# Performance work log

Hardware: AMD Instinct MI355X
Metric: run time of the kernel (lower is better)

Reference implementation:

```python
import jax, jax.numpy as jnp
import numpy as np

N = 50000      # nodes
E = 800000     # edges (avg degree 16)
D_IN = 64
D_H = 128
D_OUT = 10
EPS = 1e-8


def setup_inputs() -> dict:
    key = jax.random.key(0)
    ks = jax.random.split(key, 6)
    x = jax.random.normal(ks[0], (N, D_IN), dtype=jnp.float32)
    edge_index = jax.random.randint(ks[1], (2, E), 0, N, dtype=jnp.int32)
    # weights act on homogeneous-augmented features (d_in + 1)
    W_self0 = jax.random.normal(ks[2], (D_IN + 1, D_H), jnp.float32) / np.sqrt(D_IN + 1)
    W_neigh0 = jax.random.normal(ks[3], (D_IN + 1, D_H), jnp.float32) / np.sqrt(D_IN + 1)
    W_self1 = jax.random.normal(ks[4], (D_H + 1, D_OUT), jnp.float32) / np.sqrt(D_H + 1)
    W_neigh1 = jax.random.normal(ks[5], (D_H + 1, D_OUT), jnp.float32) / np.sqrt(D_H + 1)
    return {"x": x, "edge_index": edge_index,
            "W_self0": W_self0, "W_neigh0": W_neigh0,
            "W_self1": W_self1, "W_neigh1": W_neigh1}


def _projective_sage_layer(h, src, dst, W_self, W_neigh, last):
    n = h.shape[0]
    # lift to projective (homogeneous) coordinates: append ones column
    hh = jnp.concatenate([h, jnp.ones((n, 1), h.dtype)], axis=1)  # [N, d+1]
    # mean-aggregate neighbor messages (irregular gather + segment-sum)
    msg_sum = jax.ops.segment_sum(hh[src], dst, num_segments=n)   # [N, d+1]
    deg = jax.ops.segment_sum(jnp.ones((src.shape[0],), h.dtype), dst, num_segments=n)
    neigh = msg_sum / jnp.maximum(deg, 1.0)[:, None]
    out = hh @ W_self + neigh @ W_neigh                           # [N, d_out]
    # projective normalization (points on unit sphere of projective space)
    out = out / (jnp.linalg.norm(out, axis=1, keepdims=True) + EPS)
    return out if last else jax.nn.relu(out)


def reference(x, edge_index, W_self0, W_neigh0, W_self1, W_neigh1):
    src, dst = edge_index[0], edge_index[1]
    h = _projective_sage_layer(x, src, dst, W_self0, W_neigh0, last=False)
    h = _projective_sage_layer(h, src, dst, W_self1, W_neigh1, last=True)
    return jax.nn.log_softmax(h, axis=1)
```

## Files before the change

### kernel.cpp

```cpp
#include <hip/hip_runtime.h>
#include <hip/hip_bf16.h>
#include <math.h>

#define EPSN 1e-8f
#define MAXBUCK 512

typedef __attribute__((ext_vector_type(8))) short short8;
typedef __attribute__((ext_vector_type(4))) float f32x4;

static __device__ __forceinline__ unsigned short f2bf(float f) {
    union { float f; unsigned int u; } v; v.f = f;
    unsigned int u = v.u;
    return (unsigned short)((u + 0x7fffu + ((u >> 16) & 1u)) >> 16);
}
static __device__ __forceinline__ float bf2f(unsigned short h) {
    union { unsigned int u; float f; } v; v.u = ((unsigned int)h) << 16;
    return v.f;
}

__global__ void fused_pre(const int* __restrict__ dst, int* __restrict__ ghist, int E, int nbuck,
                          const float* __restrict__ Ws0, const float* __restrict__ Wn0,
                          const float* __restrict__ Ws1, const float* __restrict__ Wn1,
                          unsigned short* __restrict__ B0t, unsigned short* __restrict__ B1t,
                          float* __restrict__ bias,
                          const float* __restrict__ x, unsigned short* __restrict__ A0, int N,
                          int histB, int prepB) {
    int b = blockIdx.x;
    if (b < histB) {
        __shared__ int h[MAXBUCK];
        for (int i = threadIdx.x; i < MAXBUCK; i += 256) h[i] = 0;
        __syncthreads();
        int CH = (E + histB - 1) / histB;
        int lo = b * CH, hi = min(E, lo + CH);
        for (int e = lo + (int)threadIdx.x; e < hi; e += 256) atomicAdd(&h[dst[e] >> 7], 1);
        __syncthreads();
        for (int i = threadIdx.x; i < nbuck; i += 256) if (h[i]) atomicAdd(&ghist[i], h[i]);
        return;
    }
    if (b < histB + prepB) {
        int t = (b - histB) * 256 + threadIdx.x;
        if (t < 128 * 160) {
            int n = t / 160, k = t % 160;
            float v = 0.f;
            if (k < 64) v = Ws0[k * 128 + n];
            else if (k < 128) v = Wn0[(k - 64) * 128 + n];
            else if (k == 128) v = Ws0[64 * 128 + n];
            else if (k == 129) v = Wn0[64 * 128 + n];
            B0t[n * 160 + k] = f2bf(v);
        }
        int u = t - 128 * 160;
        if (u >= 0 && u < 32 * 128) {
            int c = u / 128, k = u % 128;
            float v = 0.f;
            if (c < 10) v = Ws1[k * 10 + c];
            else if (c < 20) v = Wn1[k * 10 + (c - 10)];
            B1t[c * 128 + k] = f2bf(v);
        }
        int w = t - 128 * 160 - 32 * 128;
        if (w >= 0 && w < 20) bias[w] = (w < 10) ? Ws1[128 * 10 + w] : Wn1[128 * 10 + (w - 10)];
        return;
    }
    int u = (b - histB - prepB) * 256 + threadIdx.x;
    if (u >= N * 8) return;
    int n = u >> 3, s = u & 7;
    const float4* xp = (const float4*)(x + (size_t)n * 64 + s * 8);
    float4 v0 = xp[0], v1 = xp[1];
    short8 r;
    r[0] = (short)f2bf(v0.x); r[1] = (short)f2bf(v0.y);
    r[2] = (short)f2bf(v0.z); r[3] = (short)f2bf(v0.w);
    r[4] = (short)f2bf(v1.x); r[5] = (short)f2bf(v1.y);
    r[6] = (short)f2bf(v1.z); r[7] = (short)f2bf(v1.w);
    *(short8*)(&A0[(size_t)n * 160 + s * 8]) = r;
}

__global__ void bucket_scan(const int* __restrict__ ghist, int* __restrict__ boff,
                            int* __restrict__ bcur, int nbuck, int E,
                            int* __restrict__ row_ptr, int N) {
    __shared__ int bufa[MAXBUCK], bufb[MAXBUCK];
    int t = threadIdx.x;
    int v = (t < nbuck) ? ghist[t] : 0;
    bufa[t] = v;
    __syncthreads();
    int* cur = bufa; int* nxt = bufb;
    for (int off = 1; off < MAXBUCK; off <<= 1) {
        int xv = cur[t];
        if (t >= off) xv += cur[t - off];
        nxt[t] = xv;
        __syncthreads();
        int* tmp = cur; cur = nxt; nxt = tmp;
    }
    int incl = cur[t];
    int excl = incl - v;
    if (t < nbuck) { boff[t] = excl; bcur[t] = excl; }
    if (t == nbuck - 1) boff[nbuck] = incl;
    if (t == 0) row_ptr[N] = E;
}

__global__ void bucket_scatter(const int* __restrict__ src, const int* __restrict__ dst,
                               int* __restrict__ bcur, unsigned int* __restrict__ pairs,
                               int E) {
    __shared__ int h[MAXBUCK];
    __shared__ int bs[MAXBUCK];
    for (int i = threadIdx.x; i < MAXBUCK; i += 256) h[i] = 0;
    __syncthreads();
    int CH = (E + gridDim.x - 1) / gridDim.x;
    int lo = blockIdx.x * CH, hi = min(E, lo + CH);
    for (int e = lo + (int)threadIdx.x; e < hi; e += 256) atomicAdd(&h[dst[e] >> 7], 1);
    __syncthreads();
    for (int i = threadIdx.x; i < MAXBUCK; i += 256) {
        int c = h[i];
        bs[i] = c ? atomicAdd(&bcur[i], c) : 0;
        h[i] = 0;
    }
    __syncthreads();
    for (int e = lo + (int)threadIdx.x; e < hi; e += 256) {
        int d = dst[e];
        int b = d >> 7;
        int idx = atomicAdd(&h[b], 1);
        pairs[bs[b] + idx] = (((unsigned int)(d & 127)) << 16) | (unsigned int)src[e];
    }
}

__global__ void csr_finalize(const unsigned int* __restrict__ pairs, const int* __restrict__ boff,
                             int* __restrict__ row_ptr, unsigned short* __restrict__ col,
                             int N) {
    __shared__ int lh[128], ls[128], lc[128];
    int b = blockIdx.x, t = threadIdx.x;
    int lo = boff[b], hi = boff[b + 1];
    for (int i = t; i < 128; i += 256) lh[i] = 0;
    __syncthreads();
    for (int e = lo + t; e < hi; e += 256) atomicAdd(&lh[pairs[e] >> 16], 1);
    __syncthreads();
    if (t < 128) {
        int v = lh[t];
        int incl = v;
#pragma unroll
        for (int off = 1; off < 64; off <<= 1) {
            int y = __shfl_up(incl, off);
            if ((t & 63) >= off) incl += y;
        }
        ls[t] = incl;
    }
    __syncthreads();
    if (t < 128) {
        int v = lh[t];
        int excl = ls[t] - v + ((t >= 64) ? ls[63] : 0);
        int node = b * 128 + t;
        if (node < N) row_ptr[node] = lo + excl;
        lc[t] = excl;
    }
    __syncthreads();
    for (int e = lo + t; e < hi; e += 256) {
        unsigned int p = pairs[e];
        int ld = p >> 16;
        int idx = atomicAdd(&lc[ld], 1);
        col[lo + idx] = (unsigned short)(p & 0xFFFFu);
    }
}

#define ACC4(v) { a0 += bf2f((unsigned short)((v).x & 0xFFFFu)); \
                  a1 += bf2f((unsigned short)((v).x >> 16)); \
                  a2 += bf2f((unsigned short)((v).y & 0xFFFFu)); \
                  a3 += bf2f((unsigned short)((v).y >> 16)); }

__global__ void agg0_kernel(const int* __restrict__ row_ptr, const unsigned short* __restrict__ col,
                            unsigned short* __restrict__ A0, int N) {
    int n = (int)((blockIdx.x * blockDim.x + threadIdx.x) >> 6);
    if (n >= N) return;
    int lane = threadIdx.x & 63;
    int sub = lane >> 4, f = lane & 15;
    int rs = row_ptr[n], re = row_ptr[n + 1];
    float a0 = 0.f, a1 = 0.f, a2 = 0.f, a3 = 0.f;
    for (int base = rs; base < re; base += 64) {
        int cnt = min(64, re - base);
        int e = 0;
        if (base + lane < re) e = (int)col[base + lane];
        int j = 0;
        for (; j + 16 <= cnt; j += 16) {
            int s0 = __shfl(e, j + sub);
            int s1 = __shfl(e, j + 4 + sub);
            int s2 = __shfl(e, j + 8 + sub);
            int s3 = __shfl(e, j + 12 + sub);
            uint2 v0 = *(const uint2*)(&A0[(size_t)s0 * 160 + f * 4]);
            uint2 v1 = *(const uint2*)(&A0[(size_t)s1 * 160 + f * 4]);
            uint2 v2 = *(const uint2*)(&A0[(size_t)s2 * 160 + f * 4]);
            uint2 v3 = *(const uint2*)(&A0[(size_t)s3 * 160 + f * 4]);
            ACC4(v0); ACC4(v1); ACC4(v2); ACC4(v3);
        }
        for (; j < cnt; j += 4) {
            int idx = j + sub;
            int s = __shfl(e, idx < cnt ? idx : (cnt - 1));
            if (idx < cnt) {
                uint2 v = *(const uint2*)(&A0[(size_t)s * 160 + f * 4]);
                ACC4(v);
            }
        }
    }
    a0 += __shfl_xor(a0, 16); a0 += __shfl_xor(a0, 32);
    a1 += __shfl_xor(a1, 16); a1 += __shfl_xor(a1, 32);
    a2 += __shfl_xor(a2, 16); a2 += __shfl_xor(a2, 32);
    a3 += __shfl_xor(a3, 16); a3 += __shfl_xor(a3, 32);
    float deg = (float)(re - rs);
    float scale = 1.0f / fmaxf(deg, 1.0f);
    unsigned short* row = A0 + (size_t)n * 160;
    if (sub == 0) {
        uint2 o;
        o.x = ((unsigned int)f2bf(a1 * scale) << 16) | f2bf(a0 * scale);
        o.y = ((unsigned int)f2bf(a3 * scale) << 16) | f2bf(a2 * scale);
        *(uint2*)(&row[64 + f * 4]) = o;
    } else if (sub == 1) {
        unsigned int w = (f == 0) ? ((((unsigned int)f2bf(deg * scale)) << 16) | 0x3F80u) : 0u;
        *(unsigned int*)(&row[128 + f * 2]) = w;
    }
}

__global__ void __launch_bounds__(256)
gemm0_kernel(const unsigned short* __restrict__ A0, const unsigned short* __restrict__ B0t,
             unsigned short* __restrict__ h1, int N) {
    __shared__ unsigned short As[64 * 168];
    __shared__ unsigned short Bs[128 * 168];
    int t = threadIdx.x, blk = blockIdx.x;
    for (int i = t; i < 128 * 20; i += 256) {
        int r = i / 20, c = i % 20;
        *(uint4*)(&Bs[r * 168 + c * 8]) = *(const uint4*)(&B0t[r * 160 + c * 8]);
    }
    for (int i = t; i < 64 * 20; i += 256) {
        int r = i / 20, c = i % 20;
        int gr = blk * 64 + r;
        uint4 v = {0, 0, 0, 0};
        if (gr < N) v = *(const uint4*)(&A0[(size_t)gr * 160 + c * 8]);
        *(uint4*)(&As[r * 168 + c * 8]) = v;
    }
    __syncthreads();

    int wave = t >> 6, lane = t & 63;
    int lo = lane & 15, hi = lane >> 4;
    f32x4 acc[8];
#pragma unroll
    for (int f = 0; f < 8; ++f) acc[f] = (f32x4){0.f, 0.f, 0.f, 0.f};

#pragma unroll
    for (int ks = 0; ks < 5; ++ks) {
        short8 a = *(const short8*)(&As[(wave * 16 + lo) * 168 + ks * 32 + hi * 8]);
#pragma unroll
        for (int f = 0; f < 8; ++f) {
            short8 b = *(const short8*)(&Bs[(f * 16 + lo) * 168 + ks * 32 + hi * 8]);
            acc[f] = __builtin_amdgcn_mfma_f32_16x16x32_bf16(a, b, acc[f], 0, 0, 0);
        }
    }
#pragma unroll
    for (int j = 0; j < 4; ++j) {
        float s = 0.f;
#pragma unroll
        for (int f = 0; f < 8; ++f) s += acc[f][j] * acc[f][j];
#pragma unroll
        for (int m = 1; m < 16; m <<= 1) s += __shfl_xor(s, m);
        float inv = 1.0f / (sqrtf(s) + EPSN);
        int gr = blk * 64 + wave * 16 + hi * 4 + j;
        if (gr < N) {
#pragma unroll
            for (int f = 0; f < 8; ++f)
                h1[(size_t)gr * 128 + f * 16 + lo] = f2bf(fmaxf(acc[f][j] * inv, 0.f));
        }
    }
}

__global__ void __launch_bounds__(256)
gemm1_kernel(const unsigned short* __restrict__ h1, const unsigned short* __restrict__ B1t,
             const float* __restrict__ bias, float* __restrict__ S, float* __restrict__ Qp, int N) {
    __shared__ unsigned short As[128 * 136];
    __shared__ unsigned short Bs[32 * 136];
    int t = threadIdx.x, blk = blockIdx.x;
    for (int i = t; i < 32 * 16; i += 256) {
        int r = i / 16, c = i % 16;
        *(uint4*)(&Bs[r * 136 + c * 8]) = *(const uint4*)(&B1t[r * 128 + c * 8]);
    }
    for (int i = t; i < 128 * 16; i += 256) {
        int r = i / 16, c = i % 16;
        int gr = blk * 128 + r;
        uint4 v = {0, 0, 0, 0};
        if (gr < N) v = *(const uint4*)(&h1[(size_t)gr * 128 + c * 8]);
        *(uint4*)(&As[r * 136 + c * 8]) = v;
    }
    __syncthreads();

    int wave = t >> 6, lane = t & 63, lo = lane & 15, hi = lane >> 4;
    f32x4 acc[2][2];
#pragma unroll
    for (int m = 0; m < 2; ++m) { acc[m][0] = (f32x4){0,0,0,0}; acc[m][1] = (f32x4){0,0,0,0}; }

#pragma unroll
    for (int ks = 0; ks < 4; ++ks) {
        short8 b0 = *(const short8*)(&Bs[lo * 136 + ks * 32 + hi * 8]);
        short8 b1 = *(const short8*)(&Bs[(16 + lo) * 136 + ks * 32 + hi * 8]);
#pragma unroll
        for (int m = 0; m < 2; ++m) {
            short8 a = *(const short8*)(&As[(wave * 32 + m * 16 + lo) * 136 + ks * 32 + hi * 8]);
            acc[m][0] = __builtin_amdgcn_mfma_f32_16x16x32_bf16(a, b0, acc[m][0], 0, 0, 0);
            acc[m][1] = __builtin_amdgcn_mfma_f32_16x16x32_bf16(a, b1, acc[m][1], 0, 0, 0);
        }
    }
#pragma unroll
    for (int m = 0; m < 2; ++m)
#pragma unroll
        for (int j = 0; j < 4; ++j) {
            int gr = blk * 128 + wave * 32 + m * 16 + hi * 4 + j;
            if (gr < N) {
                float v0 = acc[m][0][j] + bias[lo];
                if (lo < 10) S[(size_t)gr * 10 + lo] = v0;
                else         Qp[(size_t)gr * 16 + (lo - 10)] = v0;
                if (lo < 4)       Qp[(size_t)gr * 16 + 6 + lo] = acc[m][1][j] + bias[16 + lo];
                else if (lo < 10) Qp[(size_t)gr * 16 + 6 + lo] = 0.f;
            }
        }
}

__global__ void final_kernel(const float* __restrict__ S, const float* __restrict__ Qp,
                             const int* __restrict__ row_ptr, const unsigned short* __restrict__ col,
                             float* __restrict__ out, int N) {
    int n = (int)((blockIdx.x * blockDim.x + threadIdx.x) >> 6);
    if (n >= N) return;
    int lane = threadIdx.x & 63;
    int sub = lane >> 4, f = lane & 15;
    int rs = row_ptr[n], re = row_ptr[n + 1];
    float qx = 0.f, qy = 0.f;
    for (int base = rs; base < re; base += 64) {
        int cnt = min(64, re - base);
        int e = 0;
        if (base + lane < re) e = (int)col[base + lane];
        int j = 0;
        for (; j + 16 <= cnt; j += 16) {
            int s0 = __shfl(e, j + sub);
            int s1 = __shfl(e, j + 4 + sub);
            int s2 = __shfl(e, j + 8 + sub);
            int s3 = __shfl(e, j + 12 + sub);
            if (f < 8) {
                float2 v0 = *(const float2*)(&Qp[(size_t)s0 * 16 + f * 2]);
                float2 v1 = *(const float2*)(&Qp[(size_t)s1 * 16 + f * 2]);
                float2 v2 = *(const float2*)(&Qp[(size_t)s2 * 16 + f * 2]);
                float2 v3 = *(const float2*)(&Qp[(size_t)s3 * 16 + f * 2]);
                qx += v0.x + v1.x + v2.x + v3.x;
                qy += v0.y + v1.y + v2.y + v3.y;
            }
        }
        for (; j < cnt; j += 4) {
            int idx = j + sub;
            int s = __shfl(e, idx < cnt ? idx : (cnt - 1));
            if (idx < cnt && f < 8) {
                float2 v = *(const float2*)(&Qp[(size_t)s * 16 + f * 2]);
                qx += v.x; qy += v.y;
            }
        }
    }
    qx += __shfl_xor(qx, 16); qx += __shfl_xor(qx, 32);
    qy += __shfl_xor(qy, 16); qy += __shfl_xor(qy, 32);
    float deg = (float)(re - rs);
    float scale = 1.0f / fmaxf(deg, 1.0f);
    float px = 0.f, py = 0.f;
    if (f < 5) {
        px = S[(size_t)n * 10 + 2 * f]     + qx * scale;
        py = S[(size_t)n * 10 + 2 * f + 1] + qy * scale;
    }
    float ss = px * px + py * py;
    ss += __shfl_xor(ss, 1); ss += __shfl_xor(ss, 2);
    ss += __shfl_xor(ss, 4); ss += __shfl_xor(ss, 8);
    float inv = 1.0f / (sqrtf(ss) + EPSN);
    px *= inv; py *= inv;
    float mx = (f < 5) ? fmaxf(px, py) : -INFINITY;
    mx = fmaxf(mx, __shfl_xor(mx, 1)); mx = fmaxf(mx, __shfl_xor(mx, 2));
    mx = fmaxf(mx, __shfl_xor(mx, 4)); mx = fmaxf(mx, __shfl_xor(mx, 8));
    float se = (f < 5) ? (expf(px - mx) + expf(py - mx)) : 0.f;
    se += __shfl_xor(se, 1); se += __shfl_xor(se, 2);
    se += __shfl_xor(se, 4); se += __shfl_xor(se, 8);
    float ls = logf(se) + mx;
    if (sub == 0 && f < 5) {
        out[(size_t)n * 10 + 2 * f]     = px - ls;
        out[(size_t)n * 10 + 2 * f + 1] = py - ls;
    }
}

extern "C" void kernel_launch(void* const* d_in, const int* in_sizes, int n_in,
                              void* d_out, int out_size, void* d_ws, size_t ws_size,
                              hipStream_t stream) {
    const float* x   = (const float*)d_in[0];
    const int*   ei  = (const int*)d_in[1];
    const float* Ws0 = (const float*)d_in[2];
    const float* Wn0 = (const float*)d_in[3];
    const float* Ws1 = (const float*)d_in[4];
    const float* Wn1 = (const float*)d_in[5];

    int N = in_sizes[0] / 64;
    int E = in_sizes[1] / 2;
    const int* src = ei;
    const int* dst = ei + E;
    int nbuck = (N + 127) / 128;

    char* ws = (char*)d_ws;
    size_t off = 0;
    unsigned short* A0   = (unsigned short*)(ws + off); off += (size_t)N * 160 * 2;
    unsigned short* h1   = (unsigned short*)(ws + off); off += (size_t)N * 128 * 2;
    float*          S    = (float*)(ws + off);          off += (size_t)N * 10 * 4;
    float*          Qp   = (float*)(ws + off);          off += (size_t)N * 16 * 4;
    unsigned short* B0t  = (unsigned short*)(ws + off); off += 128 * 160 * 2;
    unsigned short* B1t  = (unsigned short*)(ws + off); off += 32 * 128 * 2;
    float*          bias = (float*)(ws + off);          off += 128;
    int*            rowp = (int*)(ws + off);            off += ((size_t)N + 4) * 4;
    unsigned short* colb = (unsigned short*)(ws + off); off += ((size_t)E + 8) * 2;
    unsigned int*   pairs= (unsigned int*)(ws + off);   off += (size_t)E * 4;
    int*            ghist= (int*)(ws + off);            off += MAXBUCK * 4;
    int*            boff = (int*)(ws + off);            off += (MAXBUCK + 1) * 4;
    int*            bcur = (int*)(ws + off);            off += MAXBUCK * 4;
    float* outp = (float*)d_out;

    int histB = 256;
    int prepB = (128 * 160 + 32 * 128 + 20 + 255) / 256;
    int xcvB  = (N * 8 + 255) / 256;

    hipMemsetAsync(ghist, 0, MAXBUCK * 4, stream);
    fused_pre<<<histB + prepB + xcvB, 256, 0, stream>>>(
        dst, ghist, E, nbuck, Ws0, Wn0, Ws1, Wn1, B0t, B1t, bias, x, A0, N, histB, prepB);
    bucket_scan   <<<1, MAXBUCK, 0, stream>>>(ghist, boff, bcur, nbuck, E, rowp, N);
    bucket_scatter<<<256, 256, 0, stream>>>(src, dst, bcur, pairs, E);
    csr_finalize  <<<nbuck, 256, 0, stream>>>(pairs, boff, rowp, colb, N);

    agg0_kernel <<<(N + 3) / 4, 256, 0, stream>>>(rowp, colb, A0, N);
    gemm0_kernel<<<(N + 63) / 64, 256, 0, stream>>>(A0, B0t, h1, N);
    gemm1_kernel<<<(N + 127) / 128, 256, 0, stream>>>(h1, B1t, bias, S, Qp, N);
    final_kernel<<<(N + 3) / 4, 256, 0, stream>>>(S, Qp, rowp, colb, outp, N);
}
```

Measured before the change: 186.7 us.

## Fuse all stages into one cooperative persistent kernel with grid syncs

Replaces the eight separate kernel launches (histogram, scan, scatter, CSR finalize, aggregation, two GEMMs, final softmax) with one cooperative kernel of 256 blocks by 512 threads that runs each stage as a grid-stride loop separated by grid.sync(). This removes the per-launch overhead and the gaps between launches. Per-stage work mappings are also reorganised, for example 8-row groups per wave in the final aggregation and split output columns with a shared-memory norm reduction in GEMM0. In exchange, parallelism is capped at 256 persistent blocks, and every grid barrier waits on the slowest block, which can leave compute units idle during the irregular gather stages.

```diff
diff --git a/kernel.cpp b/kernel.cpp
--- a/kernel.cpp
+++ b/kernel.cpp
@@ -1,9 +1,13 @@
 #include <hip/hip_runtime.h>
-#include <hip/hip_bf16.h>
+#include <hip/hip_cooperative_groups.h>
 #include <math.h>
+
+namespace cg = cooperative_groups;
 
 #define EPSN 1e-8f
 #define MAXBUCK 512
+#define NB 256
+#define NT 512
 
 typedef __attribute__((ext_vector_type(8))) short short8;
 typedef __attribute__((ext_vector_type(4))) float f32x4;
@@ -17,365 +21,367 @@
     union { unsigned int u; float f; } v; v.u = ((unsigned int)h) << 16;
     return v.f;
 }
-
-__global__ void fused_pre(const int* __restrict__ dst, int* __restrict__ ghist, int E, int nbuck,
-                          const float* __restrict__ Ws0, const float* __restrict__ Wn0,
-                          const float* __restrict__ Ws1, const float* __restrict__ Wn1,
-                          unsigned short* __restrict__ B0t, unsigned short* __restrict__ B1t,
-                          float* __restrict__ bias,
-                          const float* __restrict__ x, unsigned short* __restrict__ A0, int N,
-                          int histB, int prepB) {
-    int b = blockIdx.x;
-    if (b < histB) {
-        __shared__ int h[MAXBUCK];
-        for (int i = threadIdx.x; i < MAXBUCK; i += 256) h[i] = 0;
-        __syncthreads();
-        int CH = (E + histB - 1) / histB;
-        int lo = b * CH, hi = min(E, lo + CH);
-        for (int e = lo + (int)threadIdx.x; e < hi; e += 256) atomicAdd(&h[dst[e] >> 7], 1);
-        __syncthreads();
-        for (int i = threadIdx.x; i < nbuck; i += 256) if (h[i]) atomicAdd(&ghist[i], h[i]);
-        return;
-    }
-    if (b < histB + prepB) {
-        int t = (b - histB) * 256 + threadIdx.x;
-        if (t < 128 * 160) {
-            int n = t / 160, k = t % 160;
-            float v = 0.f;
-            if (k < 64) v = Ws0[k * 128 + n];
-            else if (k < 128) v = Wn0[(k - 64) * 128 + n];
-            else if (k == 128) v = Ws0[64 * 128 + n];
-            else if (k == 129) v = Wn0[64 * 128 + n];
-            B0t[n * 160 + k] = f2bf(v);
-        }
-        int u = t - 128 * 160;
-        if (u >= 0 && u < 32 * 128) {
-            int c = u / 128, k = u % 128;
-            float v = 0.f;
-            if (c < 10) v = Ws1[k * 10 + c];
-            else if (c < 20) v = Wn1[k * 10 + (c - 10)];
-            B1t[c * 128 + k] = f2bf(v);
-        }
-        int w = t - 128 * 160 - 32 * 128;
-        if (w >= 0 && w < 20) bias[w] = (w < 10) ? Ws1[128 * 10 + w] : Wn1[128 * 10 + (w - 10)];
-        return;
-    }
-    int u = (b - histB - prepB) * 256 + threadIdx.x;
-    if (u >= N * 8) return;
-    int n = u >> 3, s = u & 7;
-    const float4* xp = (const float4*)(x + (size_t)n * 64 + s * 8);
-    float4 v0 = xp[0], v1 = xp[1];
-    short8 r;
-    r[0] = (short)f2bf(v0.x); r[1] = (short)f2bf(v0.y);
-    r[2] = (short)f2bf(v0.z); r[3] = (short)f2bf(v0.w);
-    r[4] = (short)f2bf(v1.x); r[5] = (short)f2bf(v1.y);
-    r[6] = (short)f2bf(v1.z); r[7] = (short)f2bf(v1.w);
-    *(short8*)(&A0[(size_t)n * 160 + s * 8]) = r;
+static __device__ __forceinline__ unsigned int pk2(float a, float b) {
+    return (((unsigned int)f2bf(b)) << 16) | (unsigned int)f2bf(a);
 }
 
-__global__ void bucket_scan(const int* __restrict__ ghist, int* __restrict__ boff,
-                            int* __restrict__ bcur, int nbuck, int E,
-                            int* __restrict__ row_ptr, int N) {
-    __shared__ int bufa[MAXBUCK], bufb[MAXBUCK];
-    int t = threadIdx.x;
-    int v = (t < nbuck) ? ghist[t] : 0;
-    bufa[t] = v;
-    __syncthreads();
-    int* cur = bufa; int* nxt = bufb;
-    for (int off = 1; off < MAXBUCK; off <<= 1) {
-        int xv = cur[t];
-        if (t >= off) xv += cur[t - off];
-        nxt[t] = xv;
-        __syncthreads();
-        int* tmp = cur; cur = nxt; nxt = tmp;
-    }
-    int incl = cur[t];
-    int excl = incl - v;
-    if (t < nbuck) { boff[t] = excl; bcur[t] = excl; }
-    if (t == nbuck - 1) boff[nbuck] = incl;
-    if (t == 0) row_ptr[N] = E;
-}
-
-__global__ void bucket_scatter(const int* __restrict__ src, const int* __restrict__ dst,
-                               int* __restrict__ bcur, unsigned int* __restrict__ pairs,
-                               int E) {
-    __shared__ int h[MAXBUCK];
-    __shared__ int bs[MAXBUCK];
-    for (int i = threadIdx.x; i < MAXBUCK; i += 256) h[i] = 0;
-    __syncthreads();
-    int CH = (E + gridDim.x - 1) / gridDim.x;
-    int lo = blockIdx.x * CH, hi = min(E, lo + CH);
-    for (int e = lo + (int)threadIdx.x; e < hi; e += 256) atomicAdd(&h[dst[e] >> 7], 1);
-    __syncthreads();
-    for (int i = threadIdx.x; i < MAXBUCK; i += 256) {
-        int c = h[i];
-        bs[i] = c ? atomicAdd(&bcur[i], c) : 0;
-        h[i] = 0;
-    }
-    __syncthreads();
-    for (int e = lo + (int)threadIdx.x; e < hi; e += 256) {
-        int d = dst[e];
-        int b = d >> 7;
-        int idx = atomicAdd(&h[b], 1);
-        pairs[bs[b] + idx] = (((unsigned int)(d & 127)) << 16) | (unsigned int)src[e];
-    }
-}
-
-__global__ void csr_finalize(const unsigned int* __restrict__ pairs, const int* __restrict__ boff,
-                             int* __restrict__ row_ptr, unsigned short* __restrict__ col,
-                             int N) {
-    __shared__ int lh[128], ls[128], lc[128];
-    int b = blockIdx.x, t = threadIdx.x;
-    int lo = boff[b], hi = boff[b + 1];
-    for (int i = t; i < 128; i += 256) lh[i] = 0;
-    __syncthreads();
-    for (int e = lo + t; e < hi; e += 256) atomicAdd(&lh[pairs[e] >> 16], 1);
-    __syncthreads();
-    if (t < 128) {
-        int v = lh[t];
-        int incl = v;
-#pragma unroll
-        for (int off = 1; off < 64; off <<= 1) {
-            int y = __shfl_up(incl, off);
-            if ((t & 63) >= off) incl += y;
-        }
-        ls[t] = incl;
-    }
-    __syncthreads();
-    if (t < 128) {
-        int v = lh[t];
-        int excl = ls[t] - v + ((t >= 64) ? ls[63] : 0);
-        int node = b * 128 + t;
-        if (node < N) row_ptr[node] = lo + excl;
-        lc[t] = excl;
-    }
-    __syncthreads();
-    for (int e = lo + t; e < hi; e += 256) {
-        unsigned int p = pairs[e];
-        int ld = p >> 16;
-        int idx = atomicAdd(&lc[ld], 1);
-        col[lo + idx] = (unsigned short)(p & 0xFFFFu);
-    }
-}
-
-#define ACC4(v) { a0 += bf2f((unsigned short)((v).x & 0xFFFFu)); \
-                  a1 += bf2f((unsigned short)((v).x >> 16)); \
-                  a2 += bf2f((unsigned short)((v).y & 0xFFFFu)); \
-                  a3 += bf2f((unsigned short)((v).y >> 16)); }
-
-__global__ void agg0_kernel(const int* __restrict__ row_ptr, const unsigned short* __restrict__ col,
-                            unsigned short* __restrict__ A0, int N) {
-    int n = (int)((blockIdx.x * blockDim.x + threadIdx.x) >> 6);
-    if (n >= N) return;
-    int lane = threadIdx.x & 63;
-    int sub = lane >> 4, f = lane & 15;
-    int rs = row_ptr[n], re = row_ptr[n + 1];
-    float a0 = 0.f, a1 = 0.f, a2 = 0.f, a3 = 0.f;
-    for (int base = rs; base < re; base += 64) {
-        int cnt = min(64, re - base);
-        int e = 0;
-        if (base + lane < re) e = (int)col[base + lane];
-        int j = 0;
-        for (; j + 16 <= cnt; j += 16) {
-            int s0 = __shfl(e, j + sub);
-            int s1 = __shfl(e, j + 4 + sub);
-            int s2 = __shfl(e, j + 8 + sub);
-            int s3 = __shfl(e, j + 12 + sub);
-            uint2 v0 = *(const uint2*)(&A0[(size_t)s0 * 160 + f * 4]);
-            uint2 v1 = *(const uint2*)(&A0[(size_t)s1 * 160 + f * 4]);
-            uint2 v2 = *(const uint2*)(&A0[(size_t)s2 * 160 + f * 4]);
-            uint2 v3 = *(const uint2*)(&A0[(size_t)s3 * 160 + f * 4]);
-            ACC4(v0); ACC4(v1); ACC4(v2); ACC4(v3);
-        }
-        for (; j < cnt; j += 4) {
-            int idx = j + sub;
-            int s = __shfl(e, idx < cnt ? idx : (cnt - 1));
-            if (idx < cnt) {
-                uint2 v = *(const uint2*)(&A0[(size_t)s * 160 + f * 4]);
-                ACC4(v);
-            }
-        }
-    }
-    a0 += __shfl_xor(a0, 16); a0 += __shfl_xor(a0, 32);
-    a1 += __shfl_xor(a1, 16); a1 += __shfl_xor(a1, 32);
-    a2 += __shfl_xor(a2, 16); a2 += __shfl_xor(a2, 32);
-    a3 += __shfl_xor(a3, 16); a3 += __shfl_xor(a3, 32);
-    float deg = (float)(re - rs);
-    float scale = 1.0f / fmaxf(deg, 1.0f);
-    unsigned short* row = A0 + (size_t)n * 160;
-    if (sub == 0) {
-        uint2 o;
-        o.x = ((unsigned int)f2bf(a1 * scale) << 16) | f2bf(a0 * scale);
-        o.y = ((unsigned int)f2bf(a3 * scale) << 16) | f2bf(a2 * scale);
-        *(uint2*)(&row[64 + f * 4]) = o;
-    } else if (sub == 1) {
-        unsigned int w = (f == 0) ? ((((unsigned int)f2bf(deg * scale)) << 16) | 0x3F80u) : 0u;
-        *(unsigned int*)(&row[128 + f * 2]) = w;
-    }
-}
-
-__global__ void __launch_bounds__(256)
-gemm0_kernel(const unsigned short* __restrict__ A0, const unsigned short* __restrict__ B0t,
-             unsigned short* __restrict__ h1, int N) {
-    __shared__ unsigned short As[64 * 168];
-    __shared__ unsigned short Bs[128 * 168];
-    int t = threadIdx.x, blk = blockIdx.x;
-    for (int i = t; i < 128 * 20; i += 256) {
-        int r = i / 20, c = i % 20;
-        *(uint4*)(&Bs[r * 168 + c * 8]) = *(const uint4*)(&B0t[r * 160 + c * 8]);
-    }
-    for (int i = t; i < 64 * 20; i += 256) {
-        int r = i / 20, c = i % 20;
-        int gr = blk * 64 + r;
-        uint4 v = {0, 0, 0, 0};
-        if (gr < N) v = *(const uint4*)(&A0[(size_t)gr * 160 + c * 8]);
-        *(uint4*)(&As[r * 168 + c * 8]) = v;
-    }
-    __syncthreads();
-
-    int wave = t >> 6, lane = t & 63;
-    int lo = lane & 15, hi = lane >> 4;
-    f32x4 acc[8];
-#pragma unroll
-    for (int f = 0; f < 8; ++f) acc[f] = (f32x4){0.f, 0.f, 0.f, 0.f};
-
-#pragma unroll
-    for (int ks = 0; ks < 5; ++ks) {
-        short8 a = *(const short8*)(&As[(wave * 16 + lo) * 168 + ks * 32 + hi * 8]);
-#pragma unroll
-        for (int f = 0; f < 8; ++f) {
-            short8 b = *(const short8*)(&Bs[(f * 16 + lo) * 168 + ks * 32 + hi * 8]);
-            acc[f] = __builtin_amdgcn_mfma_f32_16x16x32_bf16(a, b, acc[f], 0, 0, 0);
-        }
-    }
-#pragma unroll
-    for (int j = 0; j < 4; ++j) {
-        float s = 0.f;
-#pragma unroll
-        for (int f = 0; f < 8; ++f) s += acc[f][j] * acc[f][j];
-#pragma unroll
-        for (int m = 1; m < 16; m <<= 1) s += __shfl_xor(s, m);
-        float inv = 1.0f / (sqrtf(s) + EPSN);
-        int gr = blk * 64 + wave * 16 + hi * 4 + j;
-        if (gr < N) {
-#pragma unroll
-            for (int f = 0; f < 8; ++f)
-                h1[(size_t)gr * 128 + f * 16 + lo] = f2bf(fmaxf(acc[f][j] * inv, 0.f));
-        }
-    }
-}
-
-__global__ void __launch_bounds__(256)
-gemm1_kernel(const unsigned short* __restrict__ h1, const unsigned short* __restrict__ B1t,
-             const float* __restrict__ bias, float* __restrict__ S, float* __restrict__ Qp, int N) {
-    __shared__ unsigned short As[128 * 136];
-    __shared__ unsigned short Bs[32 * 136];
-    int t = threadIdx.x, blk = blockIdx.x;
-    for (int i = t; i < 32 * 16; i += 256) {
-        int r = i / 16, c = i % 16;
-        *(uint4*)(&Bs[r * 136 + c * 8]) = *(const uint4*)(&B1t[r * 128 + c * 8]);
-    }
-    for (int i = t; i < 128 * 16; i += 256) {
-        int r = i / 16, c = i % 16;
-        int gr = blk * 128 + r;
-        uint4 v = {0, 0, 0, 0};
-        if (gr < N) v = *(const uint4*)(&h1[(size_t)gr * 128 + c * 8]);
-        *(uint4*)(&As[r * 136 + c * 8]) = v;
-    }
-    __syncthreads();
-
-    int wave = t >> 6, lane = t & 63, lo = lane & 15, hi = lane >> 4;
-    f32x4 acc[2][2];
-#pragma unroll
-    for (int m = 0; m < 2; ++m) { acc[m][0] = (f32x4){0,0,0,0}; acc[m][1] = (f32x4){0,0,0,0}; }
-
-#pragma unroll
-    for (int ks = 0; ks < 4; ++ks) {
-        short8 b0 = *(const short8*)(&Bs[lo * 136 + ks * 32 + hi * 8]);
-        short8 b1 = *(const short8*)(&Bs[(16 + lo) * 136 + ks * 32 + hi * 8]);
-#pragma unroll
-        for (int m = 0; m < 2; ++m) {
-            short8 a = *(const short8*)(&As[(wave * 32 + m * 16 + lo) * 136 + ks * 32 + hi * 8]);
-            acc[m][0] = __builtin_amdgcn_mfma_f32_16x16x32_bf16(a, b0, acc[m][0], 0, 0, 0);
-            acc[m][1] = __builtin_amdgcn_mfma_f32_16x16x32_bf16(a, b1, acc[m][1], 0, 0, 0);
-        }
-    }
-#pragma unroll
-    for (int m = 0; m < 2; ++m)
-#pragma unroll
-        for (int j = 0; j < 4; ++j) {
-            int gr = blk * 128 + wave * 32 + m * 16 + hi * 4 + j;
-            if (gr < N) {
-                float v0 = acc[m][0][j] + bias[lo];
-                if (lo < 10) S[(size_t)gr * 10 + lo] = v0;
-                else         Qp[(size_t)gr * 16 + (lo - 10)] = v0;
-                if (lo < 4)       Qp[(size_t)gr * 16 + 6 + lo] = acc[m][1][j] + bias[16 + lo];
-                else if (lo < 10) Qp[(size_t)gr * 16 + 6 + lo] = 0.f;
-            }
-        }
-}
-
-__global__ void final_kernel(const float* __restrict__ S, const float* __restrict__ Qp,
-                             const int* __restrict__ row_ptr, const unsigned short* __restrict__ col,
-                             float* __restrict__ out, int N) {
-    int n = (int)((blockIdx.x * blockDim.x + threadIdx.x) >> 6);
-    if (n >= N) return;
-    int lane = threadIdx.x & 63;
-    int sub = lane >> 4, f = lane & 15;
-    int rs = row_ptr[n], re = row_ptr[n + 1];
-    float qx = 0.f, qy = 0.f;
-    for (int base = rs; base < re; base += 64) {
-        int cnt = min(64, re - base);
-        int e = 0;
-        if (base + lane < re) e = (int)col[base + lane];
-        int j = 0;
-        for (; j + 16 <= cnt; j += 16) {
-            int s0 = __shfl(e, j + sub);
-            int s1 = __shfl(e, j + 4 + sub);
-            int s2 = __shfl(e, j + 8 + sub);
-            int s3 = __shfl(e, j + 12 + sub);
-            if (f < 8) {
-                float2 v0 = *(const float2*)(&Qp[(size_t)s0 * 16 + f * 2]);
-                float2 v1 = *(const float2*)(&Qp[(size_t)s1 * 16 + f * 2]);
-                float2 v2 = *(const float2*)(&Qp[(size_t)s2 * 16 + f * 2]);
-                float2 v3 = *(const float2*)(&Qp[(size_t)s3 * 16 + f * 2]);
-                qx += v0.x + v1.x + v2.x + v3.x;
-                qy += v0.y + v1.y + v2.y + v3.y;
-            }
-        }
-        for (; j < cnt; j += 4) {
-            int idx = j + sub;
-            int s = __shfl(e, idx < cnt ? idx : (cnt - 1));
-            if (idx < cnt && f < 8) {
-                float2 v = *(const float2*)(&Qp[(size_t)s * 16 + f * 2]);
-                qx += v.x; qy += v.y;
-            }
-        }
-    }
-    qx += __shfl_xor(qx, 16); qx += __shfl_xor(qx, 32);
-    qy += __shfl_xor(qy, 16); qy += __shfl_xor(qy, 32);
-    float deg = (float)(re - rs);
-    float scale = 1.0f / fmaxf(deg, 1.0f);
-    float px = 0.f, py = 0.f;
-    if (f < 5) {
-        px = S[(size_t)n * 10 + 2 * f]     + qx * scale;
-        py = S[(size_t)n * 10 + 2 * f + 1] + qy * scale;
-    }
-    float ss = px * px + py * py;
-    ss += __shfl_xor(ss, 1); ss += __shfl_xor(ss, 2);
-    ss += __shfl_xor(ss, 4); ss += __shfl_xor(ss, 8);
-    float inv = 1.0f / (sqrtf(ss) + EPSN);
-    px *= inv; py *= inv;
-    float mx = (f < 5) ? fmaxf(px, py) : -INFINITY;
-    mx = fmaxf(mx, __shfl_xor(mx, 1)); mx = fmaxf(mx, __shfl_xor(mx, 2));
-    mx = fmaxf(mx, __shfl_xor(mx, 4)); mx = fmaxf(mx, __shfl_xor(mx, 8));
-    float se = (f < 5) ? (expf(px - mx) + expf(py - mx)) : 0.f;
-    se += __shfl_xor(se, 1); se += __shfl_xor(se, 2);
-    se += __shfl_xor(se, 4); se += __shfl_xor(se, 8);
-    float ls = logf(se) + mx;
-    if (sub == 0 && f < 5) {
-        out[(size_t)n * 10 + 2 * f]     = px - ls;
-        out[(size_t)n * 10 + 2 * f + 1] = py - ls;
+struct MegaParams {
+    const float* x; const int* src; const int* dst;
+    const float* Ws0; const float* Wn0; const float* Ws1; const float* Wn1;
+    unsigned short* A0; unsigned short* h1; float* S; float* Qp;
+    unsigned short* B0t; unsigned short* B1t; float* bias;
+    int* rowp; unsigned short* colb; unsigned int* pairs;
+    int* ghist; int* boff; int* bcur;
+    float* out; int N; int E; int nbuck;
+};
+
+#define ACC8(v) { a0 += bf2f((unsigned short)((v).x & 0xFFFFu)); a1 += bf2f((unsigned short)((v).x >> 16)); \
+                  a2 += bf2f((unsigned short)((v).y & 0xFFFFu)); a3 += bf2f((unsigned short)((v).y >> 16)); \
+                  a4 += bf2f((unsigned short)((v).z & 0xFFFFu)); a5 += bf2f((unsigned short)((v).z >> 16)); \
+                  a6 += bf2f((unsigned short)((v).w & 0xFFFFu)); a7 += bf2f((unsigned short)((v).w >> 16)); }
+
+__global__ void __launch_bounds__(NT, 2) mega_kernel(MegaParams p) {
+    cg::grid_group grid = cg::this_grid();
+    __shared__ __align__(16) char smem[64512];
+    const int tid = threadIdx.x;
+    const int bid = blockIdx.x;
+    const int w = tid >> 6, lane = tid & 63;
+
+    {
+        int* h = (int*)smem;
+        for (int i = tid; i < MAXBUCK; i += NT) h[i] = 0;
+        __syncthreads();
+        int CH = (p.E + NB - 1) / NB;
+        int lo = bid * CH, hi = min(p.E, lo + CH);
+        for (int e = lo + tid; e < hi; e += NT) atomicAdd(&h[p.dst[e] >> 7], 1);
+        __syncthreads();
+        for (int i = tid; i < p.nbuck; i += NT) { int c = h[i]; if (c) atomicAdd(&p.ghist[i], c); }
+
+        for (int u = bid * NT + tid; u < p.N * 8; u += NB * NT) {
+            int n = u >> 3, s = u & 7;
+            const float4* xp = (const float4*)(p.x + (size_t)n * 64 + s * 8);
+            float4 v0 = xp[0], v1 = xp[1];
+            short8 r;
+            r[0] = (short)f2bf(v0.x); r[1] = (short)f2bf(v0.y);
+            r[2] = (short)f2bf(v0.z); r[3] = (short)f2bf(v0.w);
+            r[4] = (short)f2bf(v1.x); r[5] = (short)f2bf(v1.y);
+            r[6] = (short)f2bf(v1.z); r[7] = (short)f2bf(v1.w);
+            *(short8*)(&p.A0[(size_t)n * 160 + s * 8]) = r;
+        }
+        const int PT = 128 * 160 + 32 * 128 + 20;
+        for (int t = bid * NT + tid; t < PT; t += NB * NT) {
+            if (t < 128 * 160) {
+                int n = t / 160, k = t % 160;
+                float v = 0.f;
+                if (k < 64) v = p.Ws0[k * 128 + n];
+                else if (k < 128) v = p.Wn0[(k - 64) * 128 + n];
+                else if (k == 128) v = p.Ws0[64 * 128 + n];
+                else if (k == 129) v = p.Wn0[64 * 128 + n];
+                p.B0t[n * 160 + k] = f2bf(v);
+            } else if (t < 128 * 160 + 32 * 128) {
+                int u2 = t - 128 * 160;
+                int c = u2 / 128, k = u2 % 128;
+                float v = 0.f;
+                if (c < 10) v = p.Ws1[k * 10 + c];
+                else if (c < 20) v = p.Wn1[k * 10 + (c - 10)];
+                p.B1t[c * 128 + k] = f2bf(v);
+            } else {
+                int w2 = t - 128 * 160 - 32 * 128;
+                p.bias[w2] = (w2 < 10) ? p.Ws1[128 * 10 + w2] : p.Wn1[128 * 10 + (w2 - 10)];
+            }
+        }
+    }
+    grid.sync();
+
+    if (bid == 0) {
+        int* bufa = (int*)smem; int* bufb = bufa + MAXBUCK;
+        int t = tid;
+        int v = (t < p.nbuck) ? p.ghist[t] : 0;
+        bufa[t] = v;
+        __syncthreads();
+        int* cur = bufa; int* nxt = bufb;
+        for (int off2 = 1; off2 < MAXBUCK; off2 <<= 1) {
+            int xv = cur[t];
+            if (t >= off2) xv += cur[t - off2];
+            nxt[t] = xv;
+            __syncthreads();
+            int* tmp = cur; cur = nxt; nxt = tmp;
+        }
+        int incl = cur[t], excl = incl - v;
+        if (t < p.nbuck) { p.boff[t] = excl; p.bcur[t] = excl; }
+        if (t == p.nbuck - 1) p.boff[p.nbuck] = incl;
+        if (t == 0) p.rowp[p.N] = p.E;
+    }
+    grid.sync();
+
+    {
+        int* h = (int*)smem; int* bs = h + MAXBUCK;
+        for (int i = tid; i < MAXBUCK; i += NT) h[i] = 0;
+        __syncthreads();
+        int CH = (p.E + NB - 1) / NB;
+        int lo = bid * CH, hi = min(p.E, lo + CH);
+        for (int e = lo + tid; e < hi; e += NT) atomicAdd(&h[p.dst[e] >> 7], 1);
+        __syncthreads();
+        for (int i = tid; i < MAXBUCK; i += NT) {
+            int c = h[i];
+            bs[i] = c ? atomicAdd(&p.bcur[i], c) : 0;
+            h[i] = 0;
+        }
+        __syncthreads();
+        for (int e = lo + tid; e < hi; e += NT) {
+            int d = p.dst[e];
+            int b = d >> 7;
+            int idx = atomicAdd(&h[b], 1);
+            p.pairs[bs[b] + idx] = (((unsigned int)(d & 127)) << 16) | (unsigned int)p.src[e];
+        }
+    }
+    grid.sync();
+
+    for (int b = bid; b < p.nbuck; b += NB) {
+        int* lh = (int*)smem; int* ls = lh + 128; int* lc = ls + 128;
+        int lo = p.boff[b], hi = p.boff[b + 1];
+        for (int i = tid; i < 128; i += NT) lh[i] = 0;
+        __syncthreads();
+        for (int e = lo + tid; e < hi; e += NT) atomicAdd(&lh[p.pairs[e] >> 16], 1);
+        __syncthreads();
+        if (tid < 128) {
+            int v = lh[tid];
+            int incl = v;
+#pragma unroll
+            for (int off2 = 1; off2 < 64; off2 <<= 1) {
+                int y = __shfl_up(incl, off2);
+                if ((tid & 63) >= off2) incl += y;
+            }
+            ls[tid] = incl;
+        }
+        __syncthreads();
+        if (tid < 128) {
+            int v = lh[tid];
+            int excl = ls[tid] - v + ((tid >= 64) ? ls[63] : 0);
+            int node = b * 128 + tid;
+            if (node < p.N) p.rowp[node] = lo + excl;
+            lc[tid] = excl;
+        }
+        __syncthreads();
+        for (int e = lo + tid; e < hi; e += NT) {
+            unsigned int pr = p.pairs[e];
+            int ld = pr >> 16;
+            int idx = atomicAdd(&lc[ld], 1);
+            p.colb[lo + idx] = (unsigned short)(pr & 0xFFFFu);
+        }
+        __syncthreads();
+    }
+    grid.sync();
+
+    {
+        int sub = lane >> 3, f8 = lane & 7;
+        for (int n = bid * 8 + w; n < p.N; n += NB * 8) {
+            int rs = p.rowp[n], re = p.rowp[n + 1];
+            float a0 = 0.f, a1 = 0.f, a2 = 0.f, a3 = 0.f, a4 = 0.f, a5 = 0.f, a6 = 0.f, a7 = 0.f;
+            for (int base = rs; base < re; base += 64) {
+                int cnt = min(64, re - base);
+                int e = 0;
+                if (base + lane < re) e = (int)p.colb[base + lane];
+                int j = 0;
+                for (; j + 32 <= cnt; j += 32) {
+                    int s0 = __shfl(e, j + sub);
+                    int s1 = __shfl(e, j + 8 + sub);
+                    int s2 = __shfl(e, j + 16 + sub);
+                    int s3 = __shfl(e, j + 24 + sub);
+                    uint4 v0 = *(const uint4*)(&p.A0[(size_t)s0 * 160 + f8 * 8]);
+                    uint4 v1 = *(const uint4*)(&p.A0[(size_t)s1 * 160 + f8 * 8]);
+                    uint4 v2 = *(const uint4*)(&p.A0[(size_t)s2 * 160 + f8 * 8]);
+                    uint4 v3 = *(const uint4*)(&p.A0[(size_t)s3 * 160 + f8 * 8]);
+                    ACC8(v0); ACC8(v1); ACC8(v2); ACC8(v3);
+                }
+                for (; j < cnt; j += 8) {
+                    int idx = j + sub;
+                    int s = __shfl(e, idx < cnt ? idx : (cnt - 1));
+                    if (idx < cnt) {
+                        uint4 v = *(const uint4*)(&p.A0[(size_t)s * 160 + f8 * 8]);
+                        ACC8(v);
+                    }
+                }
+            }
+#define RED8(a) { a += __shfl_xor(a, 8); a += __shfl_xor(a, 16); a += __shfl_xor(a, 32); }
+            RED8(a0); RED8(a1); RED8(a2); RED8(a3); RED8(a4); RED8(a5); RED8(a6); RED8(a7);
+            float deg = (float)(re - rs);
+            float scale = 1.0f / fmaxf(deg, 1.0f);
+            if (sub == 0) {
+                uint4 o;
+                o.x = pk2(a0 * scale, a1 * scale);
+                o.y = pk2(a2 * scale, a3 * scale);
+                o.z = pk2(a4 * scale, a5 * scale);
+                o.w = pk2(a6 * scale, a7 * scale);
+                *(uint4*)(&p.A0[(size_t)n * 160 + 64 + f8 * 8]) = o;
+            } else if (sub == 1) {
+                uint2 z = {0u, 0u};
+                if (f8 == 0) z.x = ((unsigned int)f2bf(deg * scale) << 16) | 0x3F80u;
+                *(uint2*)(&p.A0[(size_t)n * 160 + 128 + f8 * 4]) = z;
+            }
+        }
+    }
+    grid.sync();
+
+    {
+        unsigned short* Bs = (unsigned short*)smem;
+        unsigned short* As = Bs + 128 * 168;
+        for (int i = tid; i < 128 * 20; i += NT) {
+            int r = i / 20, c = i % 20;
+            *(uint4*)(&Bs[r * 168 + c * 8]) = *(const uint4*)(&p.B0t[r * 160 + c * 8]);
+        }
+        __syncthreads();
+        int lo16 = lane & 15, hi4 = lane >> 4;
+        int rw = w >> 1, fh = w & 1;
+        int ntile = (p.N + 63) >> 6;
+        for (int tile = bid; tile < ntile; tile += NB) {
+            for (int i = tid; i < 64 * 20; i += NT) {
+                int r = i / 20, c = i % 20;
+                int gr = tile * 64 + r;
+                uint4 v = {0, 0, 0, 0};
+                if (gr < p.N) v = *(const uint4*)(&p.A0[(size_t)gr * 160 + c * 8]);
+                *(uint4*)(&As[r * 168 + c * 8]) = v;
+            }
+            __syncthreads();
+            f32x4 acc[4];
+#pragma unroll
+            for (int f = 0; f < 4; ++f) acc[f] = (f32x4){0.f, 0.f, 0.f, 0.f};
+#pragma unroll
+            for (int ks = 0; ks < 5; ++ks) {
+                short8 a = *(const short8*)(&As[(rw * 16 + lo16) * 168 + ks * 32 + hi4 * 8]);
+#pragma unroll
+                for (int f = 0; f < 4; ++f) {
+                    short8 b = *(const short8*)(&Bs[((fh * 4 + f) * 16 + lo16) * 168 + ks * 32 + hi4 * 8]);
+                    acc[f] = __builtin_amdgcn_mfma_f32_16x16x32_bf16(a, b, acc[f], 0, 0, 0);
+                }
+            }
+            __syncthreads();
+            float* sred = (float*)As;
+#pragma unroll
+            for (int j = 0; j < 4; ++j) {
+                float s = 0.f;
+#pragma unroll
+                for (int f = 0; f < 4; ++f) s += acc[f][j] * acc[f][j];
+#pragma unroll
+                for (int m = 1; m < 16; m <<= 1) s += __shfl_xor(s, m);
+                if (lo16 == 0) sred[fh * 64 + rw * 16 + hi4 * 4 + j] = s;
+            }
+            __syncthreads();
+#pragma unroll
+            for (int j = 0; j < 4; ++j) {
+                int rit = rw * 16 + hi4 * 4 + j;
+                float stot = sred[rit] + sred[64 + rit];
+                float inv = 1.0f / (sqrtf(stot) + EPSN);
+                int gr = tile * 64 + rit;
+                if (gr < p.N) {
+#pragma unroll
+                    for (int f = 0; f < 4; ++f)
+                        p.h1[(size_t)gr * 128 + (fh * 4 + f) * 16 + lo16] = f2bf(fmaxf(acc[f][j] * inv, 0.f));
+                }
+            }
+            __syncthreads();
+        }
+    }
+    grid.sync();
+
+    {
+        unsigned short* Bs = (unsigned short*)smem;
+        unsigned short* As = Bs + 32 * 136;
+        for (int i = tid; i < 32 * 16; i += NT) {
+            int r = i / 16, c = i % 16;
+            *(uint4*)(&Bs[r * 136 + c * 8]) = *(const uint4*)(&p.B1t[r * 128 + c * 8]);
+        }
+        __syncthreads();
+        int lo16 = lane & 15, hi4 = lane >> 4;
+        int ntile = (p.N + 127) >> 7;
+        for (int tile = bid; tile < ntile; tile += NB) {
+            for (int i = tid; i < 128 * 16; i += NT) {
+                int r = i / 16, c = i % 16;
+                int gr = tile * 128 + r;
+                uint4 v = {0, 0, 0, 0};
+                if (gr < p.N) v = *(const uint4*)(&p.h1[(size_t)gr * 128 + c * 8]);
+                *(uint4*)(&As[r * 136 + c * 8]) = v;
+            }
+            __syncthreads();
+            f32x4 acc0 = (f32x4){0.f, 0.f, 0.f, 0.f};
+            f32x4 acc1 = (f32x4){0.f, 0.f, 0.f, 0.f};
+#pragma unroll
+            for (int ks = 0; ks < 4; ++ks) {
+                short8 b0 = *(const short8*)(&Bs[lo16 * 136 + ks * 32 + hi4 * 8]);
+                short8 b1 = *(const short8*)(&Bs[(16 + lo16) * 136 + ks * 32 + hi4 * 8]);
+                short8 a  = *(const short8*)(&As[(w * 16 + lo16) * 136 + ks * 32 + hi4 * 8]);
+                acc0 = __builtin_amdgcn_mfma_f32_16x16x32_bf16(a, b0, acc0, 0, 0, 0);
+                acc1 = __builtin_amdgcn_mfma_f32_16x16x32_bf16(a, b1, acc1, 0, 0, 0);
+            }
+#pragma unroll
+            for (int j = 0; j < 4; ++j) {
+                int gr = tile * 128 + w * 16 + hi4 * 4 + j;
+                if (gr < p.N) {
+                    float v0 = acc0[j] + p.bias[lo16];
+                    if (lo16 < 10) p.S[(size_t)gr * 10 + lo16] = v0;
+                    else           p.Qp[(size_t)gr * 16 + (lo16 - 10)] = v0;
+                    if (lo16 < 4)       p.Qp[(size_t)gr * 16 + 6 + lo16] = acc1[j] + p.bias[16 + lo16];
+                    else if (lo16 < 10) p.Qp[(size_t)gr * 16 + 6 + lo16] = 0.f;
+                }
+            }
+            __syncthreads();
+        }
+    }
+    grid.sync();
+
+    {
+        int sub = lane >> 3, f8 = lane & 7;
+        for (int n = bid * 8 + w; n < p.N; n += NB * 8) {
+            int rs = p.rowp[n], re = p.rowp[n + 1];
+            float qx = 0.f, qy = 0.f;
+            for (int base = rs; base < re; base += 64) {
+                int cnt = min(64, re - base);
+                int e = 0;
+                if (base + lane < re) e = (int)p.colb[base + lane];
+                int j = 0;
+                for (; j + 32 <= cnt; j += 32) {
+                    int s0 = __shfl(e, j + sub);
+                    int s1 = __shfl(e, j + 8 + sub);
+                    int s2 = __shfl(e, j + 16 + sub);
+                    int s3 = __shfl(e, j + 24 + sub);
+                    float2 v0 = *(const float2*)(&p.Qp[(size_t)s0 * 16 + f8 * 2]);
+                    float2 v1 = *(const float2*)(&p.Qp[(size_t)s1 * 16 + f8 * 2]);
+                    float2 v2 = *(const float2*)(&p.Qp[(size_t)s2 * 16 + f8 * 2]);
+                    float2 v3 = *(const float2*)(&p.Qp[(size_t)s3 * 16 + f8 * 2]);
+                    qx += v0.x + v1.x + v2.x + v3.x;
+                    qy += v0.y + v1.y + v2.y + v3.y;
+                }
+                for (; j < cnt; j += 8) {
+                    int idx = j + sub;
+                    int s = __shfl(e, idx < cnt ? idx : (cnt - 1));
+                    if (idx < cnt) {
+                        float2 v = *(const float2*)(&p.Qp[(size_t)s * 16 + f8 * 2]);
+                        qx += v.x; qy += v.y;
+                    }
+                }
+            }
+            RED8(qx); RED8(qy);
+            float deg = (float)(re - rs);
+            float scale = 1.0f / fmaxf(deg, 1.0f);
+            float px = 0.f, py = 0.f;
+            if (f8 < 5) {
+                px = p.S[(size_t)n * 10 + 2 * f8]     + qx * scale;
+                py = p.S[(size_t)n * 10 + 2 * f8 + 1] + qy * scale;
+            }
+            float ss = px * px + py * py;
+            ss += __shfl_xor(ss, 1); ss += __shfl_xor(ss, 2); ss += __shfl_xor(ss, 4);
+            float inv = 1.0f / (sqrtf(ss) + EPSN);
+            px *= inv; py *= inv;
+            float mx = (f8 < 5) ? fmaxf(px, py) : -INFINITY;
+            mx = fmaxf(mx, __shfl_xor(mx, 1)); mx = fmaxf(mx, __shfl_xor(mx, 2)); mx = fmaxf(mx, __shfl_xor(mx, 4));
+            float se = (f8 < 5) ? (expf(px - mx) + expf(py - mx)) : 0.f;
+            se += __shfl_xor(se, 1); se += __shfl_xor(se, 2); se += __shfl_xor(se, 4);
+            float ls = logf(se) + mx;
+            if (sub == 0 && f8 < 5) {
+                p.out[(size_t)n * 10 + 2 * f8]     = px - ls;
+                p.out[(size_t)n * 10 + 2 * f8 + 1] = py - ls;
+            }
+        }
     }
 }
 
@@ -391,8 +397,6 @@
 
     int N = in_sizes[0] / 64;
     int E = in_sizes[1] / 2;
-    const int* src = ei;
-    const int* dst = ei + E;
     int nbuck = (N + 127) / 128;
 
     char* ws = (char*)d_ws;
@@ -410,21 +414,17 @@
     int*            ghist= (int*)(ws + off);            off += MAXBUCK * 4;
     int*            boff = (int*)(ws + off);            off += (MAXBUCK + 1) * 4;
     int*            bcur = (int*)(ws + off);            off += MAXBUCK * 4;
-    float* outp = (float*)d_out;
-
-    int histB = 256;
-    int prepB = (128 * 160 + 32 * 128 + 20 + 255) / 256;
-    int xcvB  = (N * 8 + 255) / 256;
+
+    MegaParams p;
+    p.x = x; p.src = ei; p.dst = ei + E;
+    p.Ws0 = Ws0; p.Wn0 = Wn0; p.Ws1 = Ws1; p.Wn1 = Wn1;
+    p.A0 = A0; p.h1 = h1; p.S = S; p.Qp = Qp;
+    p.B0t = B0t; p.B1t = B1t; p.bias = bias;
+    p.rowp = rowp; p.colb = colb; p.pairs = pairs;
+    p.ghist = ghist; p.boff = boff; p.bcur = bcur;
+    p.out = (float*)d_out; p.N = N; p.E = E; p.nbuck = nbuck;
 
     hipMemsetAsync(ghist, 0, MAXBUCK * 4, stream);
-    fused_pre<<<histB + prepB + xcvB, 256, 0, stream>>>(
-        dst, ghist, E, nbuck, Ws0, Wn0, Ws1, Wn1, B0t, B1t, bias, x, A0, N, histB, prepB);
-    bucket_scan   <<<1, MAXBUCK, 0, stream>>>(ghist, boff, bcur, nbuck, E, rowp, N);
-    bucket_scatter<<<256, 256, 0, stream>>>(src, dst, bcur, pairs, E);
-    csr_finalize  <<<nbuck, 256, 0, stream>>>(pairs, boff, rowp, colb, N);
-
-    agg0_kernel <<<(N + 3) / 4, 256, 0, stream>>>(rowp, colb, A0, N);
-    gemm0_kernel<<<(N + 63) / 64, 256, 0, stream>>>(A0, B0t, h1, N);
-    gemm1_kernel<<<(N + 127) / 128, 256, 0, stream>>>(h1, B1t, bias, S, Qp, N);
-    final_kernel<<<(N + 3) / 4, 256, 0, stream>>>(S, Qp, rowp, colb, outp, N);
+    void* args[] = { &p };
+    hipLaunchCooperativeKernel((const void*)mega_kernel, dim3(NB), dim3(NT), args, 0, stream);
 }
```

Measured after the change: 479.2 us. 157% more time.
